# Kernel tuning notes

Measured on AMD Instinct MI355X. Metric: run time of the kernel, lower is better.

The kernel has to match this reference:

```python
import jax, jax.numpy as jnp
import numpy as np

N_NODES = 100000
N_EDGES = 2000000
EPS = 1e-8


def setup_inputs() -> dict:
    key = jax.random.key(0)
    k1, k2 = jax.random.split(key)
    node_positions = jax.random.normal(k1, (1, N_NODES, 2), dtype=jnp.float32) * 10.0
    adjacency = jnp.zeros((1, 1, 1), dtype=jnp.float32)  # unused by this axiom
    edge_index = jax.random.randint(k2, (2, N_EDGES), 0, N_NODES, dtype=jnp.int32)
    return {"node_positions": node_positions, "adjacency": adjacency, "edge_index": edge_index}


def reference(node_positions, adjacency, edge_index):
    """OrthogonalIntegrityAxiom loss.

    Mathematically identical to enumerating all intra-node edge pairs (i<j)
    and averaging cos^2(theta)*(1-cos^2(theta)) = dot^2 - dot^4 over pairs.
    Uses the moment identity: per node n with incident unit directions d_i,
      sum_{i,j} (d_i.d_j)^2 = ||sum_i d_i (x) d_i||_F^2
      sum_{i,j} (d_i.d_j)^4 = ||sum_i d_i^{(x)4}||_F^2
    Diagonal (i=j) terms equal 1 in both sums and cancel in the difference,
    so sum_{i<j} (dot^2 - dot^4) = (S2_n - S4_n)/2.
    """
    pos = node_positions.reshape(-1, 2)                      # (N, 2)
    n_total = pos.shape[0]
    src, dst = edge_index[0], edge_index[1]
    d = pos[dst] - pos[src]                                  # (E, 2)
    d = d / jnp.maximum(jnp.linalg.norm(d, axis=-1, keepdims=True), EPS)

    # Each edge is incident to both endpoints -> 2E (node, direction) pairs.
    nodes = jnp.concatenate([src, dst])                      # (2E,)
    dirs = jnp.concatenate([d, d], axis=0)                   # (2E, 2)

    o2 = (dirs[:, :, None] * dirs[:, None, :]).reshape(-1, 4)    # d (x) d, (2E, 4)
    o4 = (o2[:, :, None] * o2[:, None, :]).reshape(-1, 16)       # d^{(x)4}, (2E, 16)

    M = jax.ops.segment_sum(o2, nodes, num_segments=n_total)     # (N, 4)
    T = jax.ops.segment_sum(o4, nodes, num_segments=n_total)     # (N, 16)
    deg = jax.ops.segment_sum(jnp.ones_like(dirs[:, 0]), nodes, num_segments=n_total)

    S2 = jnp.sum(M * M, axis=-1)   # per-node sum_{i,j} (d_i.d_j)^2
    S4 = jnp.sum(T * T, axis=-1)   # per-node sum_{i,j} (d_i.d_j)^4

    pair_loss_sum = 0.5 * jnp.sum(S2 - S4)
    n_pairs = 0.5 * jnp.sum(deg * (deg - 1.0))
    loss = pair_loss_sum / jnp.maximum(n_pairs, 1.0)
    return loss
```

## Files before the change

### kernel.cpp

```cpp
#include <hip/hip_runtime.h>
#include <math.h>

#define EPSV 1e-8f

static constexpr double QC = 1.0 / 1024.0;
static constexpr double QS = 1.0 / 512.0;

static constexpr int BLOG = 8;
static constexpr int NPB = 1 << BLOG;
static constexpr int NBIN = 512;
static constexpr int SRTN = 8192;
static constexpr int NODE_BLOCKS = 256;

__device__ __forceinline__ unsigned int make_record(float dx, float dy) {
    float n2 = dx * dx + dy * dy;
    if (n2 > EPSV * EPSV) {
        float inv = 1.0f / n2;
        float c2 = (dx * dx - dy * dy) * inv;
        float s2 = (2.0f * dx * dy) * inv;
        float c4 = c2 * c2 - s2 * s2;
        float s4 = 2.0f * c2 * s2;
        c4 = fminf(fmaxf(c4, -1.0f), 1.0f);
        s4 = fminf(fmaxf(s4, -1.0f), 1.0f);
        unsigned int c4q = (unsigned int)__float2int_rn((c4 + 1.0f) * 1024.0f);
        unsigned int s4q = (unsigned int)__float2int_rn((s4 + 1.0f) * 512.0f);
        return (c4q << 11) | s4q;
    }
    return (1u << 31) | (1024u << 11) | 512u;
}

__device__ __forceinline__ unsigned long long rec_to_val(unsigned int r) {
    return (((unsigned long long)(r >> 31)) << 60) | (1ull << 52)
         | (((unsigned long long)((r >> 11) & 0xFFFu)) << 26)
         | (unsigned long long)(r & 0x7FFu);
}

__device__ __forceinline__ void decode_accum(unsigned long long a, double& pls, double& npr) {
    double s4sum = (double)(a & 0x3FFFFFFull);
    double c4sum = (double)((a >> 26) & 0x3FFFFFFull);
    double deg = (double)((a >> 52) & 0xFFull);
    double z = (double)(a >> 60);
    double u = deg - z;
    double C = c4sum * QC - deg;
    double S = s4sum * QS - deg;
    pls += (u * u - C * C - S * S) * 0.0625;
    npr += 0.5 * deg * (deg - 1.0);
}

__global__ __launch_bounds__(256) void bin_kernel(
    const float2* __restrict__ pos,
    const int* __restrict__ ei,
    int E, int NB, int chunk, int rstride,
    unsigned short* __restrict__ ofs_out,
    unsigned int* __restrict__ buf)
{
    __shared__ unsigned int srt[SRTN];
    __shared__ unsigned int hist[512];
    __shared__ unsigned int scan[512];
    int blk = blockIdx.x;
    int t = threadIdx.x;
    int e0 = blk * chunk;
    int e1 = min(E, e0 + chunk);
    int cl = max(0, e1 - e0);
    const int* src = ei;
    const int* dst = ei + E;

    hist[t] = 0; hist[t + 256] = 0;
    __syncthreads();
    for (int e = e0 + t; e < e1; e += 256) {
        atomicAdd(&hist[src[e] >> BLOG], 1u);
        atomicAdd(&hist[dst[e] >> BLOG], 1u);
    }
    __syncthreads();
    scan[t] = hist[t]; scan[t + 256] = hist[t + 256];
    __syncthreads();
    for (int d = 1; d < 512; d <<= 1) {
        unsigned a0 = scan[t] + ((t >= d) ? scan[t - d] : 0u);
        int t2 = t + 256;
        unsigned a1 = scan[t2] + ((t2 >= d) ? scan[t2 - d] : 0u);
        __syncthreads();
        scan[t] = a0; scan[t2] = a1;
        __syncthreads();
    }
    unsigned ex0 = scan[t] - hist[t];
    unsigned ex1 = scan[t + 256] - hist[t + 256];
    size_t row = (size_t)blk * (size_t)(NB + 1);
    if (t < NB) ofs_out[row + t] = (unsigned short)ex0;
    if (t + 256 < NB) ofs_out[row + t + 256] = (unsigned short)ex1;
    if (t == 0) ofs_out[row + NB] = (unsigned short)(2 * cl);
    __syncthreads();
    hist[t] = ex0; hist[t + 256] = ex1;
    __syncthreads();
    for (int e = e0 + t; e < e1; e += 256) {
        int s = src[e], d = dst[e];
        float2 ps = pos[s], pd = pos[d];
        unsigned int rec = make_record(pd.x - ps.x, pd.y - ps.y);
        unsigned is = atomicAdd(&hist[s >> BLOG], 1u);
        srt[is] = rec | ((unsigned)(s & (NPB - 1)) << 23);
        unsigned it = atomicAdd(&hist[d >> BLOG], 1u);
        srt[it] = rec | ((unsigned)(d & (NPB - 1)) << 23);
    }
    __syncthreads();
    unsigned int* dstb = buf + (size_t)blk * (size_t)rstride;
    int nrec = 2 * cl;
    for (int i = t; i < nrec; i += 256) dstb[i] = srt[i];
}

__global__ __launch_bounds__(256) void bucket_kernel(
    const unsigned int* __restrict__ buf,
    const unsigned short* __restrict__ ofs,
    int rstride, int NB, int nbin,
    double* __restrict__ partials)
{
    __shared__ unsigned long long acc[4][NPB];
    __shared__ double sha[4], shb[4];
    int b = blockIdx.x;
    int t = threadIdx.x;
    int wid = t >> 6;
    for (int i = t; i < 4 * NPB; i += 256)
        ((unsigned long long*)acc)[i] = 0ull;
    __syncthreads();

    for (int run = t; run < nbin; run += 256) {
        size_t row = (size_t)run * (size_t)(NB + 1);
        unsigned o0 = ofs[row + b];
        unsigned o1 = ofs[row + b + 1];
        const unsigned int* p = buf + (size_t)run * (size_t)rstride + o0;
        for (unsigned i = 0; i < o1 - o0; ++i) {
            unsigned r = p[i];
            unsigned id = (r >> 23) & (NPB - 1);
            atomicAdd(&acc[wid][id], rec_to_val(r));
        }
    }
    __syncthreads();

    double pls = 0.0, npr = 0.0;
    for (int i = t; i < NPB; i += 256) {
        unsigned long long a = acc[0][i] + acc[1][i] + acc[2][i] + acc[3][i];
        decode_accum(a, pls, npr);
    }
    for (int off = 32; off > 0; off >>= 1) {
        pls += __shfl_down(pls, off, 64);
        npr += __shfl_down(npr, off, 64);
    }
    int lane = t & 63;
    if (lane == 0) { sha[wid] = pls; shb[wid] = npr; }
    __syncthreads();
    if (t == 0) {
        partials[2 * b + 0] = sha[0] + sha[1] + sha[2] + sha[3];
        partials[2 * b + 1] = shb[0] + shb[1] + shb[2] + shb[3];
    }
}

__global__ __launch_bounds__(256) void final_kernel(
    const double* __restrict__ partials,
    float* __restrict__ out,
    int nb)
{
    double pls = 0.0, npr = 0.0;
    for (int i = threadIdx.x; i < nb; i += blockDim.x) {
        pls += partials[2 * i + 0];
        npr += partials[2 * i + 1];
    }
    __shared__ double sha[4], shb[4];
    for (int off = 32; off > 0; off >>= 1) {
        pls += __shfl_down(pls, off, 64);
        npr += __shfl_down(npr, off, 64);
    }
    int lane = threadIdx.x & 63;
    int wid = threadIdx.x >> 6;
    if (lane == 0) { sha[wid] = pls; shb[wid] = npr; }
    __syncthreads();
    if (threadIdx.x == 0) {
        double a = sha[0] + sha[1] + sha[2] + sha[3];
        double b = shb[0] + shb[1] + shb[2] + shb[3];
        out[0] = (float)(a / fmax(b, 1.0));
    }
}

__global__ __launch_bounds__(256) void edge_kernel_fb(
    const float2* __restrict__ pos,
    const int* __restrict__ ei,
    unsigned long long* __restrict__ acc,
    int E)
{
    int tid = blockIdx.x * blockDim.x + threadIdx.x;
    int nthreads = gridDim.x * blockDim.x;
    const int* src = ei;
    const int* dst = ei + E;
    for (int e = tid; e < E; e += nthreads) {
        int s = src[e], t = dst[e];
        float2 ps = pos[s], pt = pos[t];
        unsigned long long val = rec_to_val(make_record(pt.x - ps.x, pt.y - ps.y));
        atomicAdd(&acc[s], val);
        atomicAdd(&acc[t], val);
    }
}

__global__ __launch_bounds__(256) void node_kernel_fb(
    const unsigned long long* __restrict__ acc,
    double* __restrict__ partials,
    int N)
{
    int tid = blockIdx.x * blockDim.x + threadIdx.x;
    int nthreads = gridDim.x * blockDim.x;
    double pls = 0.0, npr = 0.0;
    for (int n = tid; n < N; n += nthreads)
        decode_accum(acc[n], pls, npr);
    __shared__ double sha[4], shb[4];
    for (int off = 32; off > 0; off >>= 1) {
        pls += __shfl_down(pls, off, 64);
        npr += __shfl_down(npr, off, 64);
    }
    int lane = threadIdx.x & 63;
    int wid = threadIdx.x >> 6;
    if (lane == 0) { sha[wid] = pls; shb[wid] = npr; }
    __syncthreads();
    if (threadIdx.x == 0) {
        partials[2 * blockIdx.x + 0] = sha[0] + sha[1] + sha[2] + sha[3];
        partials[2 * blockIdx.x + 1] = shb[0] + shb[1] + shb[2] + shb[3];
    }
}

extern "C" void kernel_launch(void* const* d_in, const int* in_sizes, int n_in,
                              void* d_out, int out_size, void* d_ws, size_t ws_size,
                              hipStream_t stream) {
    const float* pos = (const float*)d_in[0];
    const int* ei = (const int*)d_in[2];
    int N = in_sizes[0] / 2;
    int E = in_sizes[2] / 2;
    float* out = (float*)d_out;

    int NB = (N + NPB - 1) >> BLOG;
    int chunk = (E + NBIN - 1) / NBIN;
    int nrec_max = 2 * chunk;
    int rstride = (nrec_max + 15) & ~15;

    size_t off_buf = (size_t)NB * 16;
    size_t off_ofs = off_buf + (size_t)NBIN * (size_t)rstride * 4;
    size_t need = off_ofs + (size_t)NBIN * (size_t)(NB + 1) * 2;

    if (ws_size >= need && nrec_max <= SRTN && NB + 1 <= 512 && nrec_max < 65536) {
        double* partials = (double*)d_ws;
        unsigned int* buf = (unsigned int*)((char*)d_ws + off_buf);
        unsigned short* ofs = (unsigned short*)((char*)d_ws + off_ofs);

        bin_kernel<<<NBIN, 256, 0, stream>>>(
            (const float2*)pos, ei, E, NB, chunk, rstride, ofs, buf);
        bucket_kernel<<<NB, 256, 0, stream>>>(buf, ofs, rstride, NB, NBIN, partials);
        final_kernel<<<1, 256, 0, stream>>>(partials, out, NB);
    } else {
        unsigned long long* acc = (unsigned long long*)d_ws;
        double* partials = (double*)((char*)d_ws + (size_t)N * 8);
        hipMemsetAsync(d_ws, 0, (size_t)N * 8 + (size_t)NODE_BLOCKS * 16, stream);
        int eb = min((E + 255) / 256, 2048);
        edge_kernel_fb<<<eb, 256, 0, stream>>>((const float2*)pos, ei, acc, E);
        node_kernel_fb<<<NODE_BLOCKS, 256, 0, stream>>>(acc, partials, N);
        final_kernel<<<1, 256, 0, stream>>>(partials, out, NODE_BLOCKS);
    }
}
```

Measured before the change: 114.7 us.

## Double bin count, transpose offset table, widen bucket blocks to 1024 threads

```diff
diff --git a/kernel.cpp b/kernel.cpp
--- a/kernel.cpp
+++ b/kernel.cpp
@@ -8,8 +8,9 @@
 
 static constexpr int BLOG = 8;
 static constexpr int NPB = 1 << BLOG;
-static constexpr int NBIN = 512;
-static constexpr int SRTN = 8192;
+static constexpr int NBIN = 1024;
+static constexpr int SRTN = 4096;
+static constexpr int NREP = 8;
 static constexpr int NODE_BLOCKS = 256;
 
 __device__ __forceinline__ unsigned int make_record(float dx, float dy) {
@@ -51,7 +52,7 @@
     const float2* __restrict__ pos,
     const int* __restrict__ ei,
     int E, int NB, int chunk, int rstride,
-    unsigned short* __restrict__ ofs_out,
+    unsigned short* __restrict__ ofs,
     unsigned int* __restrict__ buf)
 {
     __shared__ unsigned int srt[SRTN];
@@ -61,7 +62,6 @@
     int t = threadIdx.x;
     int e0 = blk * chunk;
     int e1 = min(E, e0 + chunk);
-    int cl = max(0, e1 - e0);
     const int* src = ei;
     const int* dst = ei + E;
 
@@ -84,10 +84,8 @@
     }
     unsigned ex0 = scan[t] - hist[t];
     unsigned ex1 = scan[t + 256] - hist[t + 256];
-    size_t row = (size_t)blk * (size_t)(NB + 1);
-    if (t < NB) ofs_out[row + t] = (unsigned short)ex0;
-    if (t + 256 < NB) ofs_out[row + t + 256] = (unsigned short)ex1;
-    if (t == 0) ofs_out[row + NB] = (unsigned short)(2 * cl);
+    if (t <= NB) ofs[(size_t)t * NBIN + blk] = (unsigned short)ex0;
+    if (t + 256 <= NB) ofs[(size_t)(t + 256) * NBIN + blk] = (unsigned short)ex1;
     __syncthreads();
     hist[t] = ex0; hist[t + 256] = ex1;
     __syncthreads();
@@ -101,54 +99,63 @@
         srt[it] = rec | ((unsigned)(d & (NPB - 1)) << 23);
     }
     __syncthreads();
-    unsigned int* dstb = buf + (size_t)blk * (size_t)rstride;
-    int nrec = 2 * cl;
-    for (int i = t; i < nrec; i += 256) dstb[i] = srt[i];
-}
-
-__global__ __launch_bounds__(256) void bucket_kernel(
+    int nrec = 2 * max(0, e1 - e0);
+    unsigned int* db = buf + (size_t)blk * (size_t)rstride;
+    int nv = nrec >> 2;
+    const uint4* s4 = (const uint4*)srt;
+    uint4* d4 = (uint4*)db;
+    for (int i = t; i < nv; i += 256) d4[i] = s4[i];
+    for (int i = (nv << 2) + t; i < nrec; i += 256) db[i] = srt[i];
+}
+
+__global__ __launch_bounds__(1024) void bucket_kernel(
     const unsigned int* __restrict__ buf,
     const unsigned short* __restrict__ ofs,
-    int rstride, int NB, int nbin,
+    int rstride,
     double* __restrict__ partials)
 {
-    __shared__ unsigned long long acc[4][NPB];
-    __shared__ double sha[4], shb[4];
+    __shared__ unsigned long long acc[NREP][NPB];
+    __shared__ unsigned short o0s[NBIN], o1s[NBIN];
+    __shared__ double sha[16], shb[16];
     int b = blockIdx.x;
     int t = threadIdx.x;
     int wid = t >> 6;
-    for (int i = t; i < 4 * NPB; i += 256)
+    for (int i = t; i < NREP * NPB; i += 1024)
         ((unsigned long long*)acc)[i] = 0ull;
-    __syncthreads();
-
-    for (int run = t; run < nbin; run += 256) {
-        size_t row = (size_t)run * (size_t)(NB + 1);
-        unsigned o0 = ofs[row + b];
-        unsigned o1 = ofs[row + b + 1];
-        const unsigned int* p = buf + (size_t)run * (size_t)rstride + o0;
-        for (unsigned i = 0; i < o1 - o0; ++i) {
+    for (int i = t; i < NBIN; i += 1024) {
+        o0s[i] = ofs[(size_t)b * NBIN + i];
+        o1s[i] = ofs[(size_t)(b + 1) * NBIN + i];
+    }
+    __syncthreads();
+
+    int rep = wid & (NREP - 1);
+    for (int run = t; run < NBIN; run += 1024) {
+        const unsigned int* p = buf + (size_t)run * (size_t)rstride;
+        int i0 = o0s[run], i1 = o1s[run];
+        for (int i = i0; i < i1; ++i) {
             unsigned r = p[i];
-            unsigned id = (r >> 23) & (NPB - 1);
-            atomicAdd(&acc[wid][id], rec_to_val(r));
+            atomicAdd(&acc[rep][(r >> 23) & (NPB - 1)], rec_to_val(r));
         }
     }
     __syncthreads();
 
     double pls = 0.0, npr = 0.0;
-    for (int i = t; i < NPB; i += 256) {
-        unsigned long long a = acc[0][i] + acc[1][i] + acc[2][i] + acc[3][i];
+    for (int i = t; i < NPB; i += 1024) {
+        unsigned long long a = 0;
+        for (int rr = 0; rr < NREP; ++rr) a += acc[rr][i];
         decode_accum(a, pls, npr);
     }
     for (int off = 32; off > 0; off >>= 1) {
         pls += __shfl_down(pls, off, 64);
         npr += __shfl_down(npr, off, 64);
     }
-    int lane = t & 63;
-    if (lane == 0) { sha[wid] = pls; shb[wid] = npr; }
+    if ((t & 63) == 0) { sha[wid] = pls; shb[wid] = npr; }
     __syncthreads();
     if (t == 0) {
-        partials[2 * b + 0] = sha[0] + sha[1] + sha[2] + sha[3];
-        partials[2 * b + 1] = shb[0] + shb[1] + shb[2] + shb[3];
+        double a = 0.0, bb = 0.0;
+        for (int i = 0; i < 16; ++i) { a += sha[i]; bb += shb[i]; }
+        partials[2 * b + 0] = a;
+        partials[2 * b + 1] = bb;
     }
 }
 
@@ -238,16 +245,16 @@
 
     size_t off_buf = (size_t)NB * 16;
     size_t off_ofs = off_buf + (size_t)NBIN * (size_t)rstride * 4;
-    size_t need = off_ofs + (size_t)NBIN * (size_t)(NB + 1) * 2;
-
-    if (ws_size >= need && nrec_max <= SRTN && NB + 1 <= 512 && nrec_max < 65536) {
+    size_t need = off_ofs + (size_t)(NB + 1) * (size_t)NBIN * 2;
+
+    if (ws_size >= need && nrec_max <= SRTN && NB + 1 <= 512) {
         double* partials = (double*)d_ws;
         unsigned int* buf = (unsigned int*)((char*)d_ws + off_buf);
         unsigned short* ofs = (unsigned short*)((char*)d_ws + off_ofs);
 
         bin_kernel<<<NBIN, 256, 0, stream>>>(
             (const float2*)pos, ei, E, NB, chunk, rstride, ofs, buf);
-        bucket_kernel<<<NB, 256, 0, stream>>>(buf, ofs, rstride, NB, NBIN, partials);
+        bucket_kernel<<<NB, 1024, 0, stream>>>(buf, ofs, rstride, partials);
         final_kernel<<<1, 256, 0, stream>>>(partials, out, NB);
     } else {
         unsigned long long* acc = (unsigned long long*)d_ws;
```

After: 136.6 us. 19.1% more time.
